# Kernel optimization log

Measured on AMD Instinct MI355X. Metric: run time of the kernel, lower is better.

## Reference

```python
import jax, jax.numpy as jnp
import numpy as np

HEADS = 8
DIM_HEAD = 64


def setup_inputs() -> dict:
    key = jax.random.key(0)
    ks = jax.random.split(key, 4)
    dim, h, w = 256, 64, 64
    hidden = HEADS * DIM_HEAD  # 512
    return {
        "x": jax.random.normal(ks[0], (dim, h, w), dtype=jnp.float32),
        "gamma": jnp.zeros((dim, 1, 1), dtype=jnp.float32),
        "mem_kv": jax.random.normal(ks[1], (2, HEADS, 4, DIM_HEAD), dtype=jnp.float32),
        "w_qkv": jax.random.normal(ks[2], (3 * hidden, dim), dtype=jnp.float32) * (dim ** -0.5),
        "w_out": jax.random.normal(ks[3], (dim, hidden), dtype=jnp.float32) * (hidden ** -0.5),
    }


def reference(x, gamma, mem_kv, w_qkv, w_out):
    c, h, w = x.shape
    scale = DIM_HEAD ** -0.5
    # RMSNorm over channel axis (axis 0), computed in fp32 like precision_cast
    xf = x.astype(jnp.float32)
    xn = (xf / jnp.linalg.norm(xf, ord=2, axis=0) * (gamma + 1.0) * (c ** 0.5)).astype(x.dtype)
    # 1x1 conv == channel matmul: (3*hidden, c) @ (c, h*w)
    qkv = jnp.einsum('oc,chw->ohw', w_qkv, xn)
    q, k, v = jnp.split(qkv, 3, axis=0)
    # '(h c) x y -> h (x y) c' with heads outermost in the channel dim
    def to_tokens(t):
        return t.reshape(HEADS, DIM_HEAD, h * w).transpose(0, 2, 1)  # [H, S, D]
    q, k, v = map(to_tokens, (q, k, v))
    k = jnp.concatenate([mem_kv[0], k], axis=-2)  # [H, M+S, D]
    v = jnp.concatenate([mem_kv[1], v], axis=-2)
    sim = jnp.einsum('hid,hjd->hij', q * scale, k)  # [H, S, M+S]
    # softmax(sim - global_max) in fp32 == stable softmax along last axis
    attn = jax.nn.softmax((sim - jnp.max(sim)).astype(jnp.float32), axis=-1).astype(sim.dtype)
    out = jnp.einsum('hij,hjd->hid', attn, v)  # [H, S, D]
    # 'h (x y) d -> (h d) x y'
    out = out.reshape(HEADS, h, w, DIM_HEAD).transpose(0, 3, 1, 2).reshape(HEADS * DIM_HEAD, h, w)
    return jnp.einsum('oc,chw->ohw', w_out, out)
```

## Files before the change

kernel.cpp:

```cpp
#include <hip/hip_runtime.h>
#include <hip/hip_bf16.h>
#include <math.h>

#define C_DIM 256
#define SPAT 4096
#define HEADS_N 8
#define DHEAD 64
#define MEMTOK 4
#define TTOK 4100
#define TTOKP 4224
#define HID 512
#define PSP 72

typedef __bf16 bf16x8 __attribute__((ext_vector_type(8)));
typedef unsigned short u16x8 __attribute__((ext_vector_type(8)));
typedef float f32x4 __attribute__((ext_vector_type(4)));

static __device__ inline unsigned short f2bf(float f) {
    unsigned int u = __float_as_uint(f);
    u += 0x7fffu + ((u >> 16) & 1u);
    return (unsigned short)(u >> 16);
}

static __device__ inline bf16x8 ldb8(const void* p) {
    union { u16x8 u; bf16x8 b; } t;
    t.u = *(const u16x8*)p;
    return t.b;
}

static __device__ inline unsigned int pkbf(float a, float b) {
    union { __bf16 h[2]; unsigned int u; } t;
    t.h[0] = (__bf16)a; t.h[1] = (__bf16)b;
    return t.u;
}

static __device__ inline int pinv(int m) {
    return (m & 3) | (((m >> 4) & 1) << 2) | (((m >> 2) & 3) << 3);
}

static __device__ inline void gload16(const void* g, void* l) {
    __builtin_amdgcn_global_load_lds(
        (const __attribute__((address_space(1))) unsigned int*)g,
        (__attribute__((address_space(3))) unsigned int*)l, 16, 0, 0);
}

#define DRAIN_BAR() do { \
    asm volatile("s_waitcnt vmcnt(0)\n\ts_barrier" ::: "memory"); \
    __builtin_amdgcn_sched_barrier(0); } while (0)

__global__ __launch_bounds__(256) void prep_kernel(
    const float* __restrict__ x, const float* __restrict__ gamma,
    const float* __restrict__ mem, const float* __restrict__ wq,
    const float* __restrict__ wo,
    unsigned short* __restrict__ xb, float* __restrict__ spb,
    unsigned short* __restrict__ wb, unsigned short* __restrict__ wob,
    unsigned short* __restrict__ kb, unsigned short* __restrict__ vtb) {
    __shared__ float XT[64][65];
    __shared__ float red[4][64];
    const int bid = blockIdx.x;
    const int t = threadIdx.x;
    if (bid < 256) {
        int p0 = (bid & 63) * 64, c0 = (bid >> 6) * 64;
#pragma unroll
        for (int i = 0; i < 4; ++i) {
            int cl = i * 16 + (t >> 4), p4 = (t & 15) * 4;
            *(float4*)&XT[cl][p4] = *(const float4*)&x[(size_t)(c0 + cl) * SPAT + p0 + p4];
        }
        __syncthreads();
        int pl = t >> 2, cs = (t & 3) * 16;
        u16x8 a, b;
#pragma unroll
        for (int j = 0; j < 8; ++j) a[j] = f2bf(XT[cs + j][pl]);
#pragma unroll
        for (int j = 0; j < 8; ++j) b[j] = f2bf(XT[cs + 8 + j][pl]);
        *(u16x8*)&xb[(size_t)(p0 + pl) * C_DIM + c0 + cs] = a;
        *(u16x8*)&xb[(size_t)(p0 + pl) * C_DIM + c0 + cs + 8] = b;
    } else if (bid < 320) {
        int p = (bid - 256) * 64 + (t & 63);
        int g = t >> 6;
        float ss = 0.f;
        for (int c = g * 64; c < g * 64 + 64; ++c) {
            float v = x[(size_t)c * SPAT + p];
            ss += v * v;
        }
        red[g][t & 63] = ss;
        __syncthreads();
        if (g == 0) {
            int lp = t & 63;
            float tot = red[0][lp] + red[1][lp] + red[2][lp] + red[3][lp];
            spb[p] = rsqrtf(tot) * 16.0f;
        }
    } else if (bid < 512) {
        size_t idx = ((size_t)(bid - 320) * 256 + t) * 8;
        int c0 = (int)(idx & 255);
        float4 f0 = *(const float4*)&wq[idx];
        float4 f1 = *(const float4*)&wq[idx + 4];
        float4 g0 = *(const float4*)&gamma[c0];
        float4 g1 = *(const float4*)&gamma[c0 + 4];
        u16x8 pk;
        pk[0] = f2bf(f0.x * (g0.x + 1.f)); pk[1] = f2bf(f0.y * (g0.y + 1.f));
        pk[2] = f2bf(f0.z * (g0.z + 1.f)); pk[3] = f2bf(f0.w * (g0.w + 1.f));
        pk[4] = f2bf(f1.x * (g1.x + 1.f)); pk[5] = f2bf(f1.y * (g1.y + 1.f));
        pk[6] = f2bf(f1.z * (g1.z + 1.f)); pk[7] = f2bf(f1.w * (g1.w + 1.f));
        *(u16x8*)&wb[idx] = pk;
    } else if (bid < 576) {
        size_t idx = ((size_t)(bid - 512) * 256 + t) * 8;
        float4 f0 = *(const float4*)&wo[idx];
        float4 f1 = *(const float4*)&wo[idx + 4];
        u16x8 pk;
        pk[0] = f2bf(f0.x); pk[1] = f2bf(f0.y); pk[2] = f2bf(f0.z); pk[3] = f2bf(f0.w);
        pk[4] = f2bf(f1.x); pk[5] = f2bf(f1.y); pk[6] = f2bf(f1.z); pk[7] = f2bf(f1.w);
        *(u16x8*)&wob[idx] = pk;
    } else {
        int i = (bid - 576) * 256 + t;
        if (i < 4096) {
            int d = i & 63, m = (i >> 6) & 3, h = (i >> 8) & 7, s = (i >> 11) & 1;
            unsigned short val = f2bf(mem[i]);
            if (s == 0) kb[(size_t)h * TTOKP * 64 + m * 64 + d] = val;
            else        vtb[((size_t)h * 64 + d) * TTOKP + m] = val;
        } else {
            int z = i - 4096;
            if (z < 63488) {
                int h = z / 7936, r = z % 7936;
                int row = TTOK + r / 64, d = r % 64;
                kb[(size_t)h * TTOKP * 64 + row * 64 + d] = 0;
            } else {
                z -= 63488;
                int h = z / 7936, r = z % 7936;
                int d = r / 124, tcol = TTOK + r % 124;
                vtb[((size_t)h * 64 + d) * TTOKP + tcol] = 0;
            }
        }
    }
}

__global__ __launch_bounds__(256) void qkv_mfma(const unsigned short* __restrict__ wb,
                                                const unsigned short* __restrict__ xb,
                                                const float* __restrict__ spb,
                                                unsigned short* __restrict__ qb,
                                                unsigned short* __restrict__ kb,
                                                unsigned short* __restrict__ vtb) {
    const int tile_p = blockIdx.x;
    const int tile_o = blockIdx.y;
    const int p0 = tile_p * 64, o0 = tile_o * 64;
    __shared__ unsigned short LB[4][64 * 128];

    const int t = threadIdx.x;
    const int w = t >> 6, lane = t & 63;
    const int col16 = lane & 15, quad = lane >> 4;
    const int c7 = col16 & 7;
    const char* gw = (const char*)(wb + (size_t)o0 * C_DIM);
    const char* gx = (const char*)(xb + (size_t)p0 * C_DIM);

    auto STG = [&](int ck, unsigned short* SWb, unsigned short* SXb) {
#pragma unroll
        for (int i = 0; i < 4; ++i) {
            int c4 = w * 4 + i;
            int row = c4 * 4 + (lane >> 4);
            int sl = (((lane & 15) ^ (row & 7)) << 4);
            size_t src = (size_t)row * 512 + ck * 256 + sl;
            gload16(gw + src, (char*)SWb + c4 * 1024);
            gload16(gx + src, (char*)SXb + c4 * 1024);
        }
    };

    f32x4 acc[4];
#pragma unroll
    for (int n = 0; n < 4; ++n) acc[n] = (f32x4){0.f, 0.f, 0.f, 0.f};
    const int arow = (w * 16 + col16) * 256;

    auto COMP = [&](const unsigned short* SWb, const unsigned short* SXb) {
#pragma unroll
        for (int kkl = 0; kkl < 4; ++kkl) {
            int ko = (((kkl * 4 + quad) ^ c7) << 4);
            bf16x8 a = ldb8((const char*)SWb + arow + ko);
#pragma unroll
            for (int n = 0; n < 4; ++n) {
                bf16x8 b = ldb8((const char*)SXb + (n * 16 + col16) * 256 + ko);
                acc[n] = __builtin_amdgcn_mfma_f32_16x16x32_bf16(a, b, acc[n], 0, 0, 0);
            }
        }
    };

    STG(0, LB[0], LB[1]);
    DRAIN_BAR();
    STG(1, LB[2], LB[3]);
    COMP(LB[0], LB[1]);
    DRAIN_BAR();
    COMP(LB[2], LB[3]);

    float spv[4];
#pragma unroll
    for (int n = 0; n < 4; ++n) spv[n] = spb[p0 + n * 16 + col16];

    const int sec = tile_o >> 3, h = tile_o & 7;
    if (sec < 2) {
        const float qsc = (sec == 0) ? 0.125f * 1.4426950408889634f : 1.0f;
        unsigned short* Ot = &LB[0][0];
        __syncthreads();
#pragma unroll
        for (int n = 0; n < 4; ++n) {
            float s = qsc * spv[n];
            ushort4 v4 = {f2bf(acc[n][0] * s), f2bf(acc[n][1] * s),
                          f2bf(acc[n][2] * s), f2bf(acc[n][3] * s)};
            *(ushort4*)&Ot[(n * 16 + col16) * PSP + w * 16 + quad * 4] = v4;
        }
        __syncthreads();
        int prow = t >> 2, dseg = t & 3;
        u16x8 va = *(u16x8*)&Ot[prow * PSP + dseg * 16];
        u16x8 vb = *(u16x8*)&Ot[prow * PSP + dseg * 16 + 8];
        unsigned short* dst = (sec == 0)
            ? qb + (size_t)h * SPAT * 64 + (size_t)(p0 + prow) * 64
            : kb + (size_t)h * TTOKP * 64 + (size_t)(MEMTOK + p0 + prow) * 64;
        *(u16x8*)&dst[dseg * 16] = va;
        *(u16x8*)&dst[dseg * 16 + 8] = vb;
    } else {
        unsigned short* dst = vtb + (size_t)h * 64 * TTOKP;
#pragma unroll
        for (int n = 0; n < 4; ++n) {
            int tg = MEMTOK + p0 + n * 16 + col16;
            int c = (tg & ~31) | pinv(tg & 31);
            float s = spv[n];
#pragma unroll
            for (int r = 0; r < 4; ++r)
                dst[(size_t)(w * 16 + quad * 4 + r) * TTOKP + c] = f2bf(acc[n][r] * s);
        }
    }
}

__global__ __launch_bounds__(256) void attn_mfma(const unsigned short* __restrict__ qb,
                                                 const unsigned short* __restrict__ kb,
                                                 const unsigned short* __restrict__ vtb,
                                                 unsigned short* __restrict__ obb) {
    const int h  = blockIdx.x & 7;
    const int p0 = (blockIdx.x >> 3) * 64;

    __shared__ unsigned short LA[4][64 * 128];

    const int t = threadIdx.x;
    const int w = t >> 6;
    const int lane = t & 63;
    const int col16 = lane & 15;
    const int quad = lane >> 4;
    const int cswz = col16 & 7;
    const int sw0 = ((quad ^ cswz) << 4);
    const int sw1 = (((quad + 4) ^ cswz) << 4);

    const unsigned short* qh = qb + (size_t)h * SPAT * 64;
    const char* khb = (const char*)(kb + (size_t)h * TTOKP * 64);
    const char* vhb = (const char*)(vtb + (size_t)h * 64 * TTOKP);

    bf16x8 aq0 = ldb8(&qh[(size_t)(p0 + w * 16 + col16) * 64 + quad * 8]);
    bf16x8 aq1 = ldb8(&qh[(size_t)(p0 + w * 16 + col16) * 64 + 32 + quad * 8]);

    float m_i = -1e30f, l_i = 0.f;
    f32x4 Oa[4];
#pragma unroll
    for (int n = 0; n < 4; ++n) Oa[n] = (f32x4){0.f, 0.f, 0.f, 0.f};

    auto STAGE = [&](int tb, unsigned short* Kd, unsigned short* Vd) {
#pragma unroll
        for (int i = 0; i < 4; ++i) {
            int ck = w * 4 + i;
            int krow = ck * 8 + (lane >> 3);
            int kcol = (((lane & 7) ^ (lane >> 3)) << 4);
            gload16(khb + (size_t)(tb * 128 + krow) * 128 + kcol, (char*)Kd + ck * 1024);
            int vrow = ck * 4 + (lane >> 4);
            int vcol = (((lane & 15) ^ (vrow & 7)) << 4);
            gload16(vhb + (size_t)vrow * (TTOKP * 2) + (size_t)tb * 256 + vcol,
                    (char*)Vd + ck * 1024);
        }
    };

    auto STEP = [&](int tile, const unsigned short* Kc_, const unsigned short* Vc_,
                    unsigned short* Ksn, unsigned short* Vsn, bool stage, bool last) {
        if (stage) STAGE(tile + 1, Ksn, Vsn);

        const char* Kc = (const char*)Kc_;
        const char* Vc = (const char*)Vc_;

        f32x4 sv[8];
#pragma unroll
        for (int n = 0; n < 8; ++n) {
            sv[n] = (f32x4){0.f, 0.f, 0.f, 0.f};
            bf16x8 bk0 = ldb8(Kc + (n * 16 + col16) * 128 + sw0);
            bf16x8 bk1 = ldb8(Kc + (n * 16 + col16) * 128 + sw1);
            sv[n] = __builtin_amdgcn_mfma_f32_16x16x32_bf16(bk0, aq0, sv[n], 0, 0, 0);
            sv[n] = __builtin_amdgcn_mfma_f32_16x16x32_bf16(bk1, aq1, sv[n], 0, 0, 0);
        }

        if (last) {
#pragma unroll
            for (int n = 0; n < 8; ++n)
#pragma unroll
                for (int r = 0; r < 4; ++r)
                    if ((n | quad) != 0) sv[n][r] = -1e30f;
        }

        float mx[8];
#pragma unroll
        for (int n = 0; n < 8; ++n)
            mx[n] = fmaxf(fmaxf(sv[n][0], sv[n][1]), fmaxf(sv[n][2], sv[n][3]));
        float rm = fmaxf(fmaxf(fmaxf(mx[0], mx[1]), fmaxf(mx[2], mx[3])),
                         fmaxf(fmaxf(mx[4], mx[5]), fmaxf(mx[6], mx[7])));
        rm = fmaxf(rm, __shfl_xor(rm, 16, 64));
        rm = fmaxf(rm, __shfl_xor(rm, 32, 64));

        float mn = fmaxf(m_i, rm);
        float al = __builtin_amdgcn_exp2f(m_i - mn);
        m_i = mn;

        float sm[8];
#pragma unroll
        for (int n = 0; n < 8; ++n) {
            float e0 = __builtin_amdgcn_exp2f(sv[n][0] - mn);
            float e1 = __builtin_amdgcn_exp2f(sv[n][1] - mn);
            float e2 = __builtin_amdgcn_exp2f(sv[n][2] - mn);
            float e3 = __builtin_amdgcn_exp2f(sv[n][3] - mn);
            sv[n][0] = e0; sv[n][1] = e1; sv[n][2] = e2; sv[n][3] = e3;
            sm[n] = (e0 + e1) + (e2 + e3);
        }
        float rs = ((sm[0] + sm[1]) + (sm[2] + sm[3])) +
                   ((sm[4] + sm[5]) + (sm[6] + sm[7]));
        rs += __shfl_xor(rs, 16, 64);
        rs += __shfl_xor(rs, 32, 64);
        l_i = l_i * al + rs;

#pragma unroll
        for (int n = 0; n < 4; ++n) {
            Oa[n][0] *= al; Oa[n][1] *= al; Oa[n][2] *= al; Oa[n][3] *= al;
        }

#pragma unroll
        for (int f = 0; f < 4; ++f) {
            union { unsigned int u[4]; bf16x8 v; } pu;
            pu.u[0] = pkbf(sv[2 * f][0], sv[2 * f][1]);
            pu.u[1] = pkbf(sv[2 * f][2], sv[2 * f][3]);
            pu.u[2] = pkbf(sv[2 * f + 1][0], sv[2 * f + 1][1]);
            pu.u[3] = pkbf(sv[2 * f + 1][2], sv[2 * f + 1][3]);
            int vo = (((f * 4 + quad) ^ cswz) << 4);
#pragma unroll
            for (int n = 0; n < 4; ++n) {
                bf16x8 bv = ldb8(Vc + (n * 16 + col16) * 256 + vo);
                Oa[n] = __builtin_amdgcn_mfma_f32_16x16x32_bf16(bv, pu.v, Oa[n], 0, 0, 0);
            }
        }

        if (!last) DRAIN_BAR();
    };

    STAGE(0, LA[0], LA[1]);
    DRAIN_BAR();
    for (int b = 0; b < 32; b += 2) {
        STEP(b,     LA[0], LA[1], LA[2], LA[3], true, false);
        STEP(b + 1, LA[2], LA[3], LA[0], LA[1], true, false);
    }
    STEP(32, LA[0], LA[1], LA[2], LA[3], false, true);

    __syncthreads();
    float inv = 1.0f / l_i;
    __bf16* ot = (__bf16*)&LA[0][0] + (size_t)w * 16 * PSP;
#pragma unroll
    for (int n = 0; n < 4; ++n) {
        *(unsigned int*)&ot[col16 * PSP + n * 16 + quad * 4] =
            pkbf(Oa[n][0] * inv, Oa[n][1] * inv);
        *(unsigned int*)&ot[col16 * PSP + n * 16 + quad * 4 + 2] =
            pkbf(Oa[n][2] * inv, Oa[n][3] * inv);
    }
    int q2 = lane >> 2, dseg = (lane & 3) * 16;
    const unsigned short* otr = (const unsigned short*)ot;
    u16x8 o0v = *(const u16x8*)&otr[q2 * PSP + dseg];
    u16x8 o1v = *(const u16x8*)&otr[q2 * PSP + dseg + 8];
    unsigned short* dst = obb + (size_t)(p0 + w * 16 + q2) * HID + h * DHEAD + dseg;
    *(u16x8*)&dst[0] = o0v;
    *(u16x8*)&dst[8] = o1v;
}

__global__ __launch_bounds__(256) void out_mfma(const unsigned short* __restrict__ wob,
                                                const unsigned short* __restrict__ obb,
                                                float* __restrict__ out) {
    const int p0 = blockIdx.x * 64;
    const int o0 = blockIdx.y * 64;
    __shared__ unsigned short LB[4][64 * 128];

    const int t = threadIdx.x;
    const int w = t >> 6, lane = t & 63;
    const int col16 = lane & 15, quad = lane >> 4;
    const int c7 = col16 & 7;
    const char* gw = (const char*)(wob + (size_t)o0 * HID);
    const char* go = (const char*)(obb + (size_t)p0 * HID);

    auto STG = [&](int ck, unsigned short* SWb, unsigned short* SOb) {
#pragma unroll
        for (int i = 0; i < 4; ++i) {
            int c4 = w * 4 + i;
            int row = c4 * 4 + (lane >> 4);
            int sl = (((lane & 15) ^ (row & 7)) << 4);
            size_t src = (size_t)row * 1024 + ck * 256 + sl;
            gload16(gw + src, (char*)SWb + c4 * 1024);
            gload16(go + src, (char*)SOb + c4 * 1024);
        }
    };

    f32x4 acc[4];
#pragma unroll
    for (int n = 0; n < 4; ++n) acc[n] = (f32x4){0.f, 0.f, 0.f, 0.f};
    const int arow = (w * 16 + col16) * 256;

    auto COMP = [&](const unsigned short* SWb, const unsigned short* SOb) {
#pragma unroll
        for (int kkl = 0; kkl < 4; ++kkl) {
            int ko = (((kkl * 4 + quad) ^ c7) << 4);
            bf16x8 a = ldb8((const char*)SWb + arow + ko);
#pragma unroll
            for (int n = 0; n < 4; ++n) {
                bf16x8 b = ldb8((const char*)SOb + (n * 16 + col16) * 256 + ko);
                acc[n] = __builtin_amdgcn_mfma_f32_16x16x32_bf16(a, b, acc[n], 0, 0, 0);
            }
        }
    };

    STG(0, LB[0], LB[1]);
    DRAIN_BAR();
    STG(1, LB[2], LB[3]);  COMP(LB[0], LB[1]);  DRAIN_BAR();
    STG(2, LB[0], LB[1]);  COMP(LB[2], LB[3]);  DRAIN_BAR();
    STG(3, LB[2], LB[3]);  COMP(LB[0], LB[1]);  DRAIN_BAR();
    COMP(LB[2], LB[3]);

    __syncthreads();
    float* otw = (float*)&LB[0][0] + (size_t)w * (16 * 68);
#pragma unroll
    for (int n = 0; n < 4; ++n)
#pragma unroll
        for (int r = 0; r < 4; ++r)
            otw[(quad * 4 + r) * 68 + n * 16 + col16] = acc[n][r];
    int r2 = lane >> 2, csg = (lane & 3) * 16;
#pragma unroll
    for (int j = 0; j < 4; ++j) {
        float4 v = *(const float4*)&otw[r2 * 68 + csg + j * 4];
        *(float4*)&out[(size_t)(o0 + w * 16 + r2) * SPAT + p0 + csg + j * 4] = v;
    }
}

extern "C" void kernel_launch(void* const* d_in, const int* in_sizes, int n_in,
                              void* d_out, int out_size, void* d_ws, size_t ws_size,
                              hipStream_t stream) {
    const float* x      = (const float*)d_in[0];
    const float* gamma  = (const float*)d_in[1];
    const float* mem_kv = (const float*)d_in[2];
    const float* w_qkv  = (const float*)d_in[3];
    const float* w_out  = (const float*)d_in[4];
    float* out = (float*)d_out;

    unsigned short* xb  = (unsigned short*)d_ws;
    unsigned short* wb  = xb + (size_t)SPAT * C_DIM;
    unsigned short* wob = wb + (size_t)3 * HID * C_DIM;
    unsigned short* qb  = wob + (size_t)C_DIM * HID;
    unsigned short* kb  = qb + (size_t)HEADS_N * SPAT * DHEAD;
    unsigned short* vtb = kb + (size_t)HEADS_N * TTOKP * DHEAD;
    unsigned short* obb = vtb + (size_t)HEADS_N * DHEAD * TTOKP;
    float* spb = (float*)(obb + (size_t)SPAT * HID);

    prep_kernel<<<dim3(1088), 256, 0, stream>>>(x, gamma, mem_kv, w_qkv, w_out,
                                                xb, spb, wb, wob, kb, vtb);
    qkv_mfma<<<dim3(64, 24), 256, 0, stream>>>(wb, xb, spb, qb, kb, vtb);
    attn_mfma<<<dim3(512), 256, 0, stream>>>(qb, kb, vtb, obb);
    out_mfma<<<dim3(64, 4), 256, 0, stream>>>(wob, obb, out);
}
```

Before: 156.9 us.

## Split attention key tiles across warp pairs and halve query rows per block

The attention kernel now processes 32 query rows per block instead of 64. Each pair of warps shares a 16-row query slice and splits each 64-key tile between them, keeping separate online-softmax state. The two partial results are merged through shared memory at the end. The grid doubles to 1024 blocks and LDS per block halves, with launch bounds requesting 4 blocks per CU, to raise occupancy and CU coverage. In exchange, K/V tiles are reloaded twice as often per query, each block runs twice as many barrier-separated steps, and there is an extra merge step.

```diff
diff --git a/kernel.cpp b/kernel.cpp
--- a/kernel.cpp
+++ b/kernel.cpp
@@ -228,20 +228,22 @@
     }
 }
 
-__global__ __launch_bounds__(256) void attn_mfma(const unsigned short* __restrict__ qb,
-                                                 const unsigned short* __restrict__ kb,
-                                                 const unsigned short* __restrict__ vtb,
-                                                 unsigned short* __restrict__ obb) {
+__global__ __launch_bounds__(256, 4) void attn_mfma(const unsigned short* __restrict__ qb,
+                                                    const unsigned short* __restrict__ kb,
+                                                    const unsigned short* __restrict__ vtb,
+                                                    unsigned short* __restrict__ obb) {
     const int h  = blockIdx.x & 7;
-    const int p0 = (blockIdx.x >> 3) * 64;
-
-    __shared__ unsigned short LA[4][64 * 128];
+    const int p0 = (blockIdx.x >> 3) * 32;
+
+    __shared__ unsigned short LA[4][64 * 64];
 
     const int t = threadIdx.x;
     const int w = t >> 6;
     const int lane = t & 63;
     const int col16 = lane & 15;
     const int quad = lane >> 4;
+    const int qsub = w & 1;
+    const int g = w >> 1;
     const int cswz = col16 & 7;
     const int sw0 = ((quad ^ cswz) << 4);
     const int sw1 = (((quad + 4) ^ cswz) << 4);
@@ -250,8 +252,8 @@
     const char* khb = (const char*)(kb + (size_t)h * TTOKP * 64);
     const char* vhb = (const char*)(vtb + (size_t)h * 64 * TTOKP);
 
-    bf16x8 aq0 = ldb8(&qh[(size_t)(p0 + w * 16 + col16) * 64 + quad * 8]);
-    bf16x8 aq1 = ldb8(&qh[(size_t)(p0 + w * 16 + col16) * 64 + 32 + quad * 8]);
+    bf16x8 aq0 = ldb8(&qh[(size_t)(p0 + qsub * 16 + col16) * 64 + quad * 8]);
+    bf16x8 aq1 = ldb8(&qh[(size_t)(p0 + qsub * 16 + col16) * 64 + 32 + quad * 8]);
 
     float m_i = -1e30f, l_i = 0.f;
     f32x4 Oa[4];
@@ -260,49 +262,44 @@
 
     auto STAGE = [&](int tb, unsigned short* Kd, unsigned short* Vd) {
 #pragma unroll
-        for (int i = 0; i < 4; ++i) {
-            int ck = w * 4 + i;
-            int krow = ck * 8 + (lane >> 3);
-            int kcol = (((lane & 7) ^ (lane >> 3)) << 4);
-            gload16(khb + (size_t)(tb * 128 + krow) * 128 + kcol, (char*)Kd + ck * 1024);
-            int vrow = ck * 4 + (lane >> 4);
-            int vcol = (((lane & 15) ^ (vrow & 7)) << 4);
-            gload16(vhb + (size_t)vrow * (TTOKP * 2) + (size_t)tb * 256 + vcol,
+        for (int i = 0; i < 2; ++i) {
+            int ck = w * 2 + i;
+            int row = ck * 8 + (lane >> 3);
+            int col = (((lane & 7) ^ (lane >> 3)) << 4);
+            gload16(khb + (size_t)(tb * 64 + row) * 128 + col, (char*)Kd + ck * 1024);
+            gload16(vhb + (size_t)row * (TTOKP * 2) + (size_t)tb * 128 + col,
                     (char*)Vd + ck * 1024);
         }
     };
 
     auto STEP = [&](int tile, const unsigned short* Kc_, const unsigned short* Vc_,
-                    unsigned short* Ksn, unsigned short* Vsn, bool stage, bool last) {
+                    unsigned short* Ksn, unsigned short* Vsn, bool stage, bool mask) {
         if (stage) STAGE(tile + 1, Ksn, Vsn);
 
         const char* Kc = (const char*)Kc_;
         const char* Vc = (const char*)Vc_;
 
-        f32x4 sv[8];
-#pragma unroll
-        for (int n = 0; n < 8; ++n) {
-            sv[n] = (f32x4){0.f, 0.f, 0.f, 0.f};
+        f32x4 sv[2];
+#pragma unroll
+        for (int nn = 0; nn < 2; ++nn) {
+            int n = g * 2 + nn;
+            sv[nn] = (f32x4){0.f, 0.f, 0.f, 0.f};
             bf16x8 bk0 = ldb8(Kc + (n * 16 + col16) * 128 + sw0);
             bf16x8 bk1 = ldb8(Kc + (n * 16 + col16) * 128 + sw1);
-            sv[n] = __builtin_amdgcn_mfma_f32_16x16x32_bf16(bk0, aq0, sv[n], 0, 0, 0);
-            sv[n] = __builtin_amdgcn_mfma_f32_16x16x32_bf16(bk1, aq1, sv[n], 0, 0, 0);
-        }
-
-        if (last) {
-#pragma unroll
-            for (int n = 0; n < 8; ++n)
+            sv[nn] = __builtin_amdgcn_mfma_f32_16x16x32_bf16(bk0, aq0, sv[nn], 0, 0, 0);
+            sv[nn] = __builtin_amdgcn_mfma_f32_16x16x32_bf16(bk1, aq1, sv[nn], 0, 0, 0);
+        }
+
+        if (mask) {
+#pragma unroll
+            for (int nn = 0; nn < 2; ++nn)
 #pragma unroll
                 for (int r = 0; r < 4; ++r)
-                    if ((n | quad) != 0) sv[n][r] = -1e30f;
-        }
-
-        float mx[8];
-#pragma unroll
-        for (int n = 0; n < 8; ++n)
-            mx[n] = fmaxf(fmaxf(sv[n][0], sv[n][1]), fmaxf(sv[n][2], sv[n][3]));
-        float rm = fmaxf(fmaxf(fmaxf(mx[0], mx[1]), fmaxf(mx[2], mx[3])),
-                         fmaxf(fmaxf(mx[4], mx[5]), fmaxf(mx[6], mx[7])));
+                    if ((g | nn | quad) != 0) sv[nn][r] = -1e30f;
+        }
+
+        float rm = fmaxf(fmaxf(fmaxf(sv[0][0], sv[0][1]), fmaxf(sv[0][2], sv[0][3])),
+                         fmaxf(fmaxf(sv[1][0], sv[1][1]), fmaxf(sv[1][2], sv[1][3])));
         rm = fmaxf(rm, __shfl_xor(rm, 16, 64));
         rm = fmaxf(rm, __shfl_xor(rm, 32, 64));
 
@@ -310,18 +307,17 @@
         float al = __builtin_amdgcn_exp2f(m_i - mn);
         m_i = mn;
 
-        float sm[8];
-#pragma unroll
-        for (int n = 0; n < 8; ++n) {
-            float e0 = __builtin_amdgcn_exp2f(sv[n][0] - mn);
-            float e1 = __builtin_amdgcn_exp2f(sv[n][1] - mn);
-            float e2 = __builtin_amdgcn_exp2f(sv[n][2] - mn);
-            float e3 = __builtin_amdgcn_exp2f(sv[n][3] - mn);
-            sv[n][0] = e0; sv[n][1] = e1; sv[n][2] = e2; sv[n][3] = e3;
-            sm[n] = (e0 + e1) + (e2 + e3);
-        }
-        float rs = ((sm[0] + sm[1]) + (sm[2] + sm[3])) +
-                   ((sm[4] + sm[5]) + (sm[6] + sm[7]));
+        float sm[2];
+#pragma unroll
+        for (int nn = 0; nn < 2; ++nn) {
+            float e0 = __builtin_amdgcn_exp2f(sv[nn][0] - mn);
+            float e1 = __builtin_amdgcn_exp2f(sv[nn][1] - mn);
+            float e2 = __builtin_amdgcn_exp2f(sv[nn][2] - mn);
+            float e3 = __builtin_amdgcn_exp2f(sv[nn][3] - mn);
+            sv[nn][0] = e0; sv[nn][1] = e1; sv[nn][2] = e2; sv[nn][3] = e3;
+            sm[nn] = (e0 + e1) + (e2 + e3);
+        }
+        float rs = sm[0] + sm[1];
         rs += __shfl_xor(rs, 16, 64);
         rs += __shfl_xor(rs, 32, 64);
         l_i = l_i * al + rs;
@@ -331,49 +327,69 @@
             Oa[n][0] *= al; Oa[n][1] *= al; Oa[n][2] *= al; Oa[n][3] *= al;
         }
 
-#pragma unroll
-        for (int f = 0; f < 4; ++f) {
-            union { unsigned int u[4]; bf16x8 v; } pu;
-            pu.u[0] = pkbf(sv[2 * f][0], sv[2 * f][1]);
-            pu.u[1] = pkbf(sv[2 * f][2], sv[2 * f][3]);
-            pu.u[2] = pkbf(sv[2 * f + 1][0], sv[2 * f + 1][1]);
-            pu.u[3] = pkbf(sv[2 * f + 1][2], sv[2 * f + 1][3]);
-            int vo = (((f * 4 + quad) ^ cswz) << 4);
-#pragma unroll
-            for (int n = 0; n < 4; ++n) {
-                bf16x8 bv = ldb8(Vc + (n * 16 + col16) * 256 + vo);
-                Oa[n] = __builtin_amdgcn_mfma_f32_16x16x32_bf16(bv, pu.v, Oa[n], 0, 0, 0);
-            }
-        }
-
-        if (!last) DRAIN_BAR();
+        union { unsigned int u[4]; bf16x8 v; } pu;
+        pu.u[0] = pkbf(sv[0][0], sv[0][1]);
+        pu.u[1] = pkbf(sv[0][2], sv[0][3]);
+        pu.u[2] = pkbf(sv[1][0], sv[1][1]);
+        pu.u[3] = pkbf(sv[1][2], sv[1][3]);
+        int vo = (((g * 4 + quad) ^ cswz) << 4);
+#pragma unroll
+        for (int n = 0; n < 4; ++n) {
+            bf16x8 bv = ldb8(Vc + (n * 16 + col16) * 128 + vo);
+            Oa[n] = __builtin_amdgcn_mfma_f32_16x16x32_bf16(bv, pu.v, Oa[n], 0, 0, 0);
+        }
+
+        if (!mask) DRAIN_BAR();
     };
 
     STAGE(0, LA[0], LA[1]);
     DRAIN_BAR();
-    for (int b = 0; b < 32; b += 2) {
+    for (int b = 0; b < 64; b += 2) {
         STEP(b,     LA[0], LA[1], LA[2], LA[3], true, false);
         STEP(b + 1, LA[2], LA[3], LA[0], LA[1], true, false);
     }
-    STEP(32, LA[0], LA[1], LA[2], LA[3], false, true);
+    STEP(64, LA[0], LA[1], LA[2], LA[3], false, true);
 
     __syncthreads();
-    float inv = 1.0f / l_i;
-    __bf16* ot = (__bf16*)&LA[0][0] + (size_t)w * 16 * PSP;
-#pragma unroll
-    for (int n = 0; n < 4; ++n) {
-        *(unsigned int*)&ot[col16 * PSP + n * 16 + quad * 4] =
-            pkbf(Oa[n][0] * inv, Oa[n][1] * inv);
-        *(unsigned int*)&ot[col16 * PSP + n * 16 + quad * 4 + 2] =
-            pkbf(Oa[n][2] * inv, Oa[n][3] * inv);
-    }
-    int q2 = lane >> 2, dseg = (lane & 3) * 16;
-    const unsigned short* otr = (const unsigned short*)ot;
-    u16x8 o0v = *(const u16x8*)&otr[q2 * PSP + dseg];
-    u16x8 o1v = *(const u16x8*)&otr[q2 * PSP + dseg + 8];
-    unsigned short* dst = obb + (size_t)(p0 + w * 16 + q2) * HID + h * DHEAD + dseg;
-    *(u16x8*)&dst[0] = o0v;
-    *(u16x8*)&dst[8] = o1v;
+    float* MB = (float*)&LA[0][0];
+    float2* ML = (float2*)((char*)&LA[0][0] + 8704);
+    __bf16* TR = (__bf16*)&LA[2][0];
+
+    if (g == 1) {
+        float* row = MB + (qsub * 16 + col16) * 68;
+#pragma unroll
+        for (int n = 0; n < 4; ++n)
+#pragma unroll
+            for (int r = 0; r < 4; ++r)
+                row[n * 16 + quad * 4 + r] = Oa[n][r];
+        if (quad == 0) ML[qsub * 16 + col16] = make_float2(m_i, l_i);
+    }
+    __syncthreads();
+    if (g == 0) {
+        float2 o = ML[qsub * 16 + col16];
+        float M = fmaxf(m_i, o.x);
+        float a0 = __builtin_amdgcn_exp2f(m_i - M);
+        float a1 = __builtin_amdgcn_exp2f(o.x - M);
+        float inv = 1.0f / (a0 * l_i + a1 * o.y);
+        const float* row = MB + (qsub * 16 + col16) * 68;
+        __bf16* ot = TR + (size_t)qsub * 16 * PSP;
+#pragma unroll
+        for (int n = 0; n < 4; ++n) {
+            float v0 = (a0 * Oa[n][0] + a1 * row[n * 16 + quad * 4 + 0]) * inv;
+            float v1 = (a0 * Oa[n][1] + a1 * row[n * 16 + quad * 4 + 1]) * inv;
+            float v2 = (a0 * Oa[n][2] + a1 * row[n * 16 + quad * 4 + 2]) * inv;
+            float v3 = (a0 * Oa[n][3] + a1 * row[n * 16 + quad * 4 + 3]) * inv;
+            *(unsigned int*)&ot[col16 * PSP + n * 16 + quad * 4]     = pkbf(v0, v1);
+            *(unsigned int*)&ot[col16 * PSP + n * 16 + quad * 4 + 2] = pkbf(v2, v3);
+        }
+        int q2 = lane >> 2, dseg = (lane & 3) * 16;
+        const unsigned short* otr = (const unsigned short*)ot;
+        u16x8 o0v = *(const u16x8*)&otr[q2 * PSP + dseg];
+        u16x8 o1v = *(const u16x8*)&otr[q2 * PSP + dseg + 8];
+        unsigned short* dst = obb + (size_t)(p0 + qsub * 16 + q2) * HID + h * DHEAD + dseg;
+        *(u16x8*)&dst[0] = o0v;
+        *(u16x8*)&dst[8] = o1v;
+    }
 }
 
 __global__ __launch_bounds__(256) void out_mfma(const unsigned short* __restrict__ wob,
@@ -464,6 +480,6 @@
     prep_kernel<<<dim3(1088), 256, 0, stream>>>(x, gamma, mem_kv, w_qkv, w_out,
                                                 xb, spb, wb, wob, kb, vtb);
     qkv_mfma<<<dim3(64, 24), 256, 0, stream>>>(wb, xb, spb, qb, kb, vtb);
-    attn_mfma<<<dim3(512), 256, 0, stream>>>(qb, kb, vtb, obb);
+    attn_mfma<<<dim3(1024), 256, 0, stream>>>(qb, kb, vtb, obb);
     out_mfma<<<dim3(64, 4), 256, 0, stream>>>(wob, obb, out);
 }
```

After: 170.7 us. 8.8% more time.

## Split attention KV tile across wave pairs with two query sub-tiles per wave

Applied to the files above, without the earlier changes.

Each wave now processes two 16-row query sub-tiles against half of each 128-token KV tile, so K and V fragments read from LDS are reused across two query blocks. Each wave pair keeps separate online-softmax states, which are merged through shared memory at the end before the bf16 output is written. This cuts LDS traffic per MFMA. In exchange it roughly doubles accumulator register use, adds a cross-wave merge step, and runs more shuffle reductions per step.

```diff
diff --git a/kernel.cpp b/kernel.cpp
--- a/kernel.cpp
+++ b/kernel.cpp
@@ -242,6 +242,8 @@
     const int lane = t & 63;
     const int col16 = lane & 15;
     const int quad = lane >> 4;
+    const int qsub = w >> 1;
+    const int kh = w & 1;
     const int cswz = col16 & 7;
     const int sw0 = ((quad ^ cswz) << 4);
     const int sw1 = (((quad + 4) ^ cswz) << 4);
@@ -250,13 +252,20 @@
     const char* khb = (const char*)(kb + (size_t)h * TTOKP * 64);
     const char* vhb = (const char*)(vtb + (size_t)h * 64 * TTOKP);
 
-    bf16x8 aq0 = ldb8(&qh[(size_t)(p0 + w * 16 + col16) * 64 + quad * 8]);
-    bf16x8 aq1 = ldb8(&qh[(size_t)(p0 + w * 16 + col16) * 64 + 32 + quad * 8]);
-
-    float m_i = -1e30f, l_i = 0.f;
-    f32x4 Oa[4];
-#pragma unroll
-    for (int n = 0; n < 4; ++n) Oa[n] = (f32x4){0.f, 0.f, 0.f, 0.f};
+    bf16x8 aq0[2], aq1[2];
+#pragma unroll
+    for (int qq = 0; qq < 2; ++qq) {
+        const unsigned short* qr = &qh[(size_t)(p0 + qsub * 32 + qq * 16 + col16) * 64];
+        aq0[qq] = ldb8(qr + quad * 8);
+        aq1[qq] = ldb8(qr + 32 + quad * 8);
+    }
+
+    float m_i[2] = {-1e30f, -1e30f}, l_i[2] = {0.f, 0.f};
+    f32x4 Oa[2][4];
+#pragma unroll
+    for (int qq = 0; qq < 2; ++qq)
+#pragma unroll
+        for (int n = 0; n < 4; ++n) Oa[qq][n] = (f32x4){0.f, 0.f, 0.f, 0.f};
 
     auto STAGE = [&](int tb, unsigned short* Kd, unsigned short* Vd) {
 #pragma unroll
@@ -273,80 +282,95 @@
     };
 
     auto STEP = [&](int tile, const unsigned short* Kc_, const unsigned short* Vc_,
-                    unsigned short* Ksn, unsigned short* Vsn, bool stage, bool last) {
+                    unsigned short* Ksn, unsigned short* Vsn, bool stage, bool mask) {
         if (stage) STAGE(tile + 1, Ksn, Vsn);
 
         const char* Kc = (const char*)Kc_;
         const char* Vc = (const char*)Vc_;
 
-        f32x4 sv[8];
-#pragma unroll
-        for (int n = 0; n < 8; ++n) {
-            sv[n] = (f32x4){0.f, 0.f, 0.f, 0.f};
-            bf16x8 bk0 = ldb8(Kc + (n * 16 + col16) * 128 + sw0);
-            bf16x8 bk1 = ldb8(Kc + (n * 16 + col16) * 128 + sw1);
-            sv[n] = __builtin_amdgcn_mfma_f32_16x16x32_bf16(bk0, aq0, sv[n], 0, 0, 0);
-            sv[n] = __builtin_amdgcn_mfma_f32_16x16x32_bf16(bk1, aq1, sv[n], 0, 0, 0);
-        }
-
-        if (last) {
-#pragma unroll
-            for (int n = 0; n < 8; ++n)
-#pragma unroll
-                for (int r = 0; r < 4; ++r)
-                    if ((n | quad) != 0) sv[n][r] = -1e30f;
-        }
-
-        float mx[8];
-#pragma unroll
-        for (int n = 0; n < 8; ++n)
-            mx[n] = fmaxf(fmaxf(sv[n][0], sv[n][1]), fmaxf(sv[n][2], sv[n][3]));
-        float rm = fmaxf(fmaxf(fmaxf(mx[0], mx[1]), fmaxf(mx[2], mx[3])),
-                         fmaxf(fmaxf(mx[4], mx[5]), fmaxf(mx[6], mx[7])));
-        rm = fmaxf(rm, __shfl_xor(rm, 16, 64));
-        rm = fmaxf(rm, __shfl_xor(rm, 32, 64));
-
-        float mn = fmaxf(m_i, rm);
-        float al = __builtin_amdgcn_exp2f(m_i - mn);
-        m_i = mn;
-
-        float sm[8];
-#pragma unroll
-        for (int n = 0; n < 8; ++n) {
-            float e0 = __builtin_amdgcn_exp2f(sv[n][0] - mn);
-            float e1 = __builtin_amdgcn_exp2f(sv[n][1] - mn);
-            float e2 = __builtin_amdgcn_exp2f(sv[n][2] - mn);
-            float e3 = __builtin_amdgcn_exp2f(sv[n][3] - mn);
-            sv[n][0] = e0; sv[n][1] = e1; sv[n][2] = e2; sv[n][3] = e3;
-            sm[n] = (e0 + e1) + (e2 + e3);
-        }
-        float rs = ((sm[0] + sm[1]) + (sm[2] + sm[3])) +
-                   ((sm[4] + sm[5]) + (sm[6] + sm[7]));
-        rs += __shfl_xor(rs, 16, 64);
-        rs += __shfl_xor(rs, 32, 64);
-        l_i = l_i * al + rs;
-
-#pragma unroll
-        for (int n = 0; n < 4; ++n) {
-            Oa[n][0] *= al; Oa[n][1] *= al; Oa[n][2] *= al; Oa[n][3] *= al;
-        }
-
-#pragma unroll
-        for (int f = 0; f < 4; ++f) {
-            union { unsigned int u[4]; bf16x8 v; } pu;
-            pu.u[0] = pkbf(sv[2 * f][0], sv[2 * f][1]);
-            pu.u[1] = pkbf(sv[2 * f][2], sv[2 * f][3]);
-            pu.u[2] = pkbf(sv[2 * f + 1][0], sv[2 * f + 1][1]);
-            pu.u[3] = pkbf(sv[2 * f + 1][2], sv[2 * f + 1][3]);
-            int vo = (((f * 4 + quad) ^ cswz) << 4);
+        f32x4 sv[2][4];
+#pragma unroll
+        for (int nn = 0; nn < 4; ++nn) {
+            int krow = kh * 64 + nn * 16 + col16;
+            bf16x8 bk0 = ldb8(Kc + krow * 128 + sw0);
+            bf16x8 bk1 = ldb8(Kc + krow * 128 + sw1);
+#pragma unroll
+            for (int qq = 0; qq < 2; ++qq) {
+                f32x4 z = (f32x4){0.f, 0.f, 0.f, 0.f};
+                z = __builtin_amdgcn_mfma_f32_16x16x32_bf16(bk0, aq0[qq], z, 0, 0, 0);
+                sv[qq][nn] = __builtin_amdgcn_mfma_f32_16x16x32_bf16(bk1, aq1[qq], z, 0, 0, 0);
+            }
+        }
+
+        if (mask) {
+#pragma unroll
+            for (int qq = 0; qq < 2; ++qq)
+#pragma unroll
+                for (int nn = 0; nn < 4; ++nn)
+#pragma unroll
+                    for (int r = 0; r < 4; ++r)
+                        if ((kh | nn | quad) != 0) sv[qq][nn][r] = -1e30f;
+        }
+
+        float al[2];
+#pragma unroll
+        for (int qq = 0; qq < 2; ++qq) {
+            float rm = fmaxf(
+                fmaxf(fmaxf(sv[qq][0][0], sv[qq][0][1]), fmaxf(sv[qq][0][2], sv[qq][0][3])),
+                fmaxf(fmaxf(sv[qq][1][0], sv[qq][1][1]), fmaxf(sv[qq][1][2], sv[qq][1][3])));
+            rm = fmaxf(rm, fmaxf(
+                fmaxf(fmaxf(sv[qq][2][0], sv[qq][2][1]), fmaxf(sv[qq][2][2], sv[qq][2][3])),
+                fmaxf(fmaxf(sv[qq][3][0], sv[qq][3][1]), fmaxf(sv[qq][3][2], sv[qq][3][3]))));
+            rm = fmaxf(rm, __shfl_xor(rm, 16, 64));
+            rm = fmaxf(rm, __shfl_xor(rm, 32, 64));
+            float mn = fmaxf(m_i[qq], rm);
+            al[qq] = __builtin_amdgcn_exp2f(m_i[qq] - mn);
+            m_i[qq] = mn;
+            float sm[4];
+#pragma unroll
+            for (int nn = 0; nn < 4; ++nn) {
+                float e0 = __builtin_amdgcn_exp2f(sv[qq][nn][0] - mn);
+                float e1 = __builtin_amdgcn_exp2f(sv[qq][nn][1] - mn);
+                float e2 = __builtin_amdgcn_exp2f(sv[qq][nn][2] - mn);
+                float e3 = __builtin_amdgcn_exp2f(sv[qq][nn][3] - mn);
+                sv[qq][nn][0] = e0; sv[qq][nn][1] = e1;
+                sv[qq][nn][2] = e2; sv[qq][nn][3] = e3;
+                sm[nn] = (e0 + e1) + (e2 + e3);
+            }
+            float rs = (sm[0] + sm[1]) + (sm[2] + sm[3]);
+            rs += __shfl_xor(rs, 16, 64);
+            rs += __shfl_xor(rs, 32, 64);
+            l_i[qq] = l_i[qq] * al[qq] + rs;
 #pragma unroll
             for (int n = 0; n < 4; ++n) {
-                bf16x8 bv = ldb8(Vc + (n * 16 + col16) * 256 + vo);
-                Oa[n] = __builtin_amdgcn_mfma_f32_16x16x32_bf16(bv, pu.v, Oa[n], 0, 0, 0);
-            }
-        }
-
-        if (!last) DRAIN_BAR();
+                Oa[qq][n][0] *= al[qq]; Oa[qq][n][1] *= al[qq];
+                Oa[qq][n][2] *= al[qq]; Oa[qq][n][3] *= al[qq];
+            }
+        }
+
+#pragma unroll
+        for (int ff = 0; ff < 2; ++ff) {
+            int F = kh * 2 + ff;
+            int vo = (((F * 4 + quad) ^ cswz) << 4);
+            bf16x8 bv[4];
+#pragma unroll
+            for (int n = 0; n < 4; ++n)
+                bv[n] = ldb8(Vc + (n * 16 + col16) * 256 + vo);
+#pragma unroll
+            for (int qq = 0; qq < 2; ++qq) {
+                union { unsigned int u[4]; bf16x8 v; } pu;
+                pu.u[0] = pkbf(sv[qq][2 * ff][0], sv[qq][2 * ff][1]);
+                pu.u[1] = pkbf(sv[qq][2 * ff][2], sv[qq][2 * ff][3]);
+                pu.u[2] = pkbf(sv[qq][2 * ff + 1][0], sv[qq][2 * ff + 1][1]);
+                pu.u[3] = pkbf(sv[qq][2 * ff + 1][2], sv[qq][2 * ff + 1][3]);
+#pragma unroll
+                for (int n = 0; n < 4; ++n)
+                    Oa[qq][n] = __builtin_amdgcn_mfma_f32_16x16x32_bf16(bv[n], pu.v,
+                                                                        Oa[qq][n], 0, 0, 0);
+            }
+        }
+
+        if (!mask) DRAIN_BAR();
     };
 
     STAGE(0, LA[0], LA[1]);
@@ -358,22 +382,57 @@
     STEP(32, LA[0], LA[1], LA[2], LA[3], false, true);
 
     __syncthreads();
-    float inv = 1.0f / l_i;
-    __bf16* ot = (__bf16*)&LA[0][0] + (size_t)w * 16 * PSP;
-#pragma unroll
-    for (int n = 0; n < 4; ++n) {
-        *(unsigned int*)&ot[col16 * PSP + n * 16 + quad * 4] =
-            pkbf(Oa[n][0] * inv, Oa[n][1] * inv);
-        *(unsigned int*)&ot[col16 * PSP + n * 16 + quad * 4 + 2] =
-            pkbf(Oa[n][2] * inv, Oa[n][3] * inv);
-    }
-    int q2 = lane >> 2, dseg = (lane & 3) * 16;
-    const unsigned short* otr = (const unsigned short*)ot;
-    u16x8 o0v = *(const u16x8*)&otr[q2 * PSP + dseg];
-    u16x8 o1v = *(const u16x8*)&otr[q2 * PSP + dseg + 8];
-    unsigned short* dst = obb + (size_t)(p0 + w * 16 + q2) * HID + h * DHEAD + dseg;
-    *(u16x8*)&dst[0] = o0v;
-    *(u16x8*)&dst[8] = o1v;
+    float* MB = (float*)&LA[0][0];
+    float2* ML = (float2*)((char*)&LA[0][0] + 64 * 68 * 4);
+    __bf16* TR = (__bf16*)&LA[2][0];
+
+    if (kh == 1) {
+#pragma unroll
+        for (int qq = 0; qq < 2; ++qq) {
+            float* row = MB + (qsub * 32 + qq * 16 + col16) * 68;
+#pragma unroll
+            for (int n = 0; n < 4; ++n)
+#pragma unroll
+                for (int r = 0; r < 4; ++r)
+                    row[n * 16 + quad * 4 + r] = Oa[qq][n][r];
+            if (quad == 0)
+                ML[qsub * 32 + qq * 16 + col16] = make_float2(m_i[qq], l_i[qq]);
+        }
+    }
+    __syncthreads();
+    if (kh == 0) {
+#pragma unroll
+        for (int qq = 0; qq < 2; ++qq) {
+            float2 o = ML[qsub * 32 + qq * 16 + col16];
+            float M = fmaxf(m_i[qq], o.x);
+            float a0 = __builtin_amdgcn_exp2f(m_i[qq] - M);
+            float a1 = __builtin_amdgcn_exp2f(o.x - M);
+            float inv = 1.0f / (a0 * l_i[qq] + a1 * o.y);
+            const float* row = MB + (qsub * 32 + qq * 16 + col16) * 68;
+            __bf16* ot = TR + (size_t)(qsub * 32 + qq * 16) * PSP;
+#pragma unroll
+            for (int n = 0; n < 4; ++n) {
+                float v0 = (a0 * Oa[qq][n][0] + a1 * row[n * 16 + quad * 4 + 0]) * inv;
+                float v1 = (a0 * Oa[qq][n][1] + a1 * row[n * 16 + quad * 4 + 1]) * inv;
+                float v2 = (a0 * Oa[qq][n][2] + a1 * row[n * 16 + quad * 4 + 2]) * inv;
+                float v3 = (a0 * Oa[qq][n][3] + a1 * row[n * 16 + quad * 4 + 3]) * inv;
+                *(unsigned int*)&ot[col16 * PSP + n * 16 + quad * 4]     = pkbf(v0, v1);
+                *(unsigned int*)&ot[col16 * PSP + n * 16 + quad * 4 + 2] = pkbf(v2, v3);
+            }
+        }
+        int q2 = lane >> 2, dseg = (lane & 3) * 16;
+#pragma unroll
+        for (int qq = 0; qq < 2; ++qq) {
+            const unsigned short* otr =
+                (const unsigned short*)(TR + (size_t)(qsub * 32 + qq * 16) * PSP);
+            u16x8 o0v = *(const u16x8*)&otr[q2 * PSP + dseg];
+            u16x8 o1v = *(const u16x8*)&otr[q2 * PSP + dseg + 8];
+            unsigned short* dst = obb +
+                (size_t)(p0 + qsub * 32 + qq * 16 + q2) * HID + h * DHEAD + dseg;
+            *(u16x8*)&dst[0] = o0v;
+            *(u16x8*)&dst[8] = o1v;
+        }
+    }
 }
 
 __global__ __launch_bounds__(256) void out_mfma(const unsigned short* __restrict__ wob,
```

Result: slower. 177.6 us (+13.2%).
